# Kernel tuning notes

Hardware: AMD Instinct MI355X
Metric: run time of the kernel (lower is better)

The kernel has to match this reference:

```python
import jax, jax.numpy as jnp
import numpy as np

D_MODEL = 256
N_LAYER = 4
D_INNER = 512   # expand=2
D_STATE = 16
DT_RANK = 16    # ceil(d_model/16)
D_CONV = 4
VOCAB = 16
BATCH = 1
SEQLEN = 4096
EPS = 1e-5


def setup_inputs() -> dict:
    key = jax.random.key(0)
    ks = jax.random.split(key, 10)
    s = 0.02
    A_init = jnp.log(jnp.arange(1, D_STATE + 1, dtype=jnp.float32))  # S4D-real init
    return {
        "input_ids": jax.random.randint(ks[0], (BATCH, SEQLEN), 0, VOCAB, dtype=jnp.int32),
        "embed_w": jax.random.normal(ks[1], (VOCAB, D_MODEL), jnp.float32) * s,
        "norm_w": jnp.ones((N_LAYER, D_MODEL), jnp.float32),
        "in_proj_w": jax.random.normal(ks[2], (N_LAYER, 2 * D_INNER, D_MODEL), jnp.float32) * s,
        "out_proj_w": jax.random.normal(ks[3], (N_LAYER, D_MODEL, D_INNER), jnp.float32) * s,
        "conv_w": jax.random.normal(ks[4], (N_LAYER, 2, D_INNER, D_CONV), jnp.float32) * s,
        "conv_b": jnp.zeros((N_LAYER, 2, D_INNER), jnp.float32),
        "x_proj_w": jax.random.normal(ks[5], (N_LAYER, 2, DT_RANK + 2 * D_STATE, D_INNER), jnp.float32) * s,
        "dt_proj_w": jax.random.normal(ks[6], (N_LAYER, 2, D_INNER, DT_RANK), jnp.float32) * s,
        "dt_proj_b": jax.random.normal(ks[7], (N_LAYER, 2, D_INNER), jnp.float32) * 0.1,
        "A_log": jnp.broadcast_to(A_init, (N_LAYER, 2, D_INNER, D_STATE)) + 0.0,
        "Dp": jnp.ones((N_LAYER, 2, D_INNER), jnp.float32),
        "norm_f_w": jnp.ones((D_MODEL,), jnp.float32),
    }


def rmsnorm(x, w):
    return x * jax.lax.rsqrt(jnp.mean(x * x, axis=-1, keepdims=True) + EPS) * w


def selective_scan(u, dt, A, Bm, Cm, Dv):
    # u, dt: (B,L,Di); A: (Di,N); Bm, Cm: (B,L,N); Dv: (Di,)
    dA = jnp.exp(dt[..., None] * A)                         # (B,L,Di,N)
    dBu = dt[..., None] * Bm[:, :, None, :] * u[..., None]  # (B,L,Di,N)

    def step(h, xs):
        dA_t, dBu_t, C_t = xs
        h = dA_t * h + dBu_t                                # (B,Di,N)
        y = jnp.einsum('bdn,bn->bd', h, C_t)
        return h, y

    h0 = jnp.zeros((u.shape[0], D_INNER, D_STATE), u.dtype)
    xs = (jnp.moveaxis(dA, 1, 0), jnp.moveaxis(dBu, 1, 0), jnp.moveaxis(Cm, 1, 0))
    _, ys = jax.lax.scan(step, h0, xs)                      # (L,B,Di)
    return jnp.moveaxis(ys, 0, 1) + u * Dv


def mamba_dir(x, in_w, out_w, cw, cb, xpw, dtw, dtb, a_log, dv):
    # x: (B,L,D)
    xz = jnp.einsum('bld,ed->ble', x, in_w)                 # (B,L,2*Di)
    u, z = jnp.split(xz, 2, axis=-1)
    # causal depthwise conv1d
    uc = jnp.moveaxis(u, 1, 2)                              # (B,Di,L)
    uc = jax.lax.conv_general_dilated(
        uc, cw[:, None, :], (1,), [(D_CONV - 1, 0)],
        feature_group_count=D_INNER, dimension_numbers=('NCH', 'OIH', 'NCH'))
    u = jax.nn.silu(jnp.moveaxis(uc, 1, 2) + cb)            # (B,L,Di)
    xdb = jnp.einsum('bld,ed->ble', u, xpw)                 # (B,L,dt_rank+2N)
    dt_r, Bm, Cm = jnp.split(xdb, [DT_RANK, DT_RANK + D_STATE], axis=-1)
    dt = jax.nn.softplus(jnp.einsum('blr,dr->bld', dt_r, dtw) + dtb)
    A = -jnp.exp(a_log)                                     # (Di,N)
    y = selective_scan(u, dt, A, Bm, Cm, dv)
    y = y * jax.nn.silu(z)
    return jnp.einsum('bld,od->blo', y, out_w)


def reference(input_ids, embed_w, norm_w, in_proj_w, out_proj_w, conv_w, conv_b,
              x_proj_w, dt_proj_w, dt_proj_b, A_log, Dp, norm_f_w):
    h = embed_w[input_ids]                                  # (B,L,D)
    residual = None
    for i in range(N_LAYER):
        residual = h if residual is None else h + residual  # residual_in_fp32
        hn = rmsnorm(residual, norm_w[i])
        out_f = mamba_dir(hn, in_proj_w[i], out_proj_w[i], conv_w[i, 0], conv_b[i, 0],
                          x_proj_w[i, 0], dt_proj_w[i, 0], dt_proj_b[i, 0], A_log[i, 0], Dp[i, 0])
        out_r = mamba_dir(hn[:, ::-1], in_proj_w[i], out_proj_w[i], conv_w[i, 1], conv_b[i, 1],
                          x_proj_w[i, 1], dt_proj_w[i, 1], dt_proj_b[i, 1], A_log[i, 1], Dp[i, 1])[:, ::-1]
        h = out_f + out_r                                   # bidirectional 'add'
    residual = h + residual
    return rmsnorm(residual, norm_f_w)
```

## Files before the change

### kernel.cpp

```cpp
#include <hip/hip_runtime.h>
#include <hip/hip_bf16.h>
#include <math.h>

#define L_  4096
#define D_  256
#define DI_ 512
#define NS_ 16
#define NC_ 128
#define CH_ 32

typedef __attribute__((ext_vector_type(8))) short short8;
typedef __attribute__((ext_vector_type(4))) short short4v;
typedef __attribute__((ext_vector_type(4))) float f32x4;

__global__ __launch_bounds__(256) void prep_kernel(const int* __restrict__ ids,
    const float* __restrict__ ew, const float* __restrict__ inw,
    const float* __restrict__ outw, const float* __restrict__ xpw,
    float* __restrict__ res, __hip_bfloat16* __restrict__ inw_b,
    __hip_bfloat16* __restrict__ outw_b, __hip_bfloat16* __restrict__ xpw_b) {
  int idx = blockIdx.x * 256 + threadIdx.x;
  int l = idx >> 8, d = idx & 255;
  res[idx] = ew[ids[l] * D_ + d];
  inw_b[idx] = __float2bfloat16(inw[idx]);
  if (idx < 4 * 256 * 512)
    outw_b[idx] = __float2bfloat16(outw[idx]);
  if (idx < 4 * 2 * 64 * 512) {
    int layer = idx >> 16;
    int rem = idx & 65535;
    int dir = rem >> 15;
    int r = (rem >> 9) & 63, k = idx & 511;
    float v = (r < 48) ? xpw[(((size_t)layer * 2 + dir) * 48 + r) * 512 + k] : 0.f;
    xpw_b[idx] = __float2bfloat16(v);
  }
}

template<bool BF16OUT>
__global__ __launch_bounds__(256) void rmsnorm_kernel(float* __restrict__ residual,
    const float* __restrict__ h0, const float* __restrict__ h1,
    const float* __restrict__ w, void* __restrict__ out) {
  int row = blockIdx.x * 4 + (threadIdx.x >> 6);
  int lane = threadIdx.x & 63;
  size_t o = (size_t)row * D_ + lane * 4;
  float4 v = *(const float4*)(residual + o);
  if (h0) {
    float4 a = *(const float4*)(h0 + o);
    float4 b = *(const float4*)(h1 + o);
    v.x += a.x + b.x; v.y += a.y + b.y; v.z += a.z + b.z; v.w += a.w + b.w;
    *(float4*)(residual + o) = v;
  }
  float sq = fmaf(v.x, v.x, fmaf(v.y, v.y, fmaf(v.z, v.z, v.w * v.w)));
  #pragma unroll
  for (int s = 32; s > 0; s >>= 1) sq += __shfl_xor(sq, s, 64);
  float scale = rsqrtf(sq * (1.f / D_) + 1e-5f);
  float4 wv = *(const float4*)(w + lane * 4);
  float r0 = v.x * scale * wv.x, r1 = v.y * scale * wv.y;
  float r2 = v.z * scale * wv.z, r3 = v.w * scale * wv.w;
  if (BF16OUT) {
    __hip_bfloat16* ob = (__hip_bfloat16*)out + o;
    short4v s4;
    s4[0] = __bfloat16_as_short(__float2bfloat16(r0));
    s4[1] = __bfloat16_as_short(__float2bfloat16(r1));
    s4[2] = __bfloat16_as_short(__float2bfloat16(r2));
    s4[3] = __bfloat16_as_short(__float2bfloat16(r3));
    *reinterpret_cast<short4v*>(ob) = s4;
  } else {
    float4 r = {r0, r1, r2, r3};
    *((float4*)out + (o >> 2)) = r;
  }
}

__device__ __forceinline__ void gload_lds16(const void* g, void* l) {
  __builtin_amdgcn_global_load_lds((const __attribute__((address_space(1))) unsigned int*)g,
                                   (__attribute__((address_space(3))) unsigned int*)l,
                                   16, 0, 0);
}

template<int BM, int BN, bool BF16OUT>
__global__ __launch_bounds__(256) void gemm_bt_bf16(const __hip_bfloat16* __restrict__ A,
    const __hip_bfloat16* __restrict__ B, void* __restrict__ Cv, int M, int N, int K,
    size_t sA, size_t sB, size_t sC) {
  A += (size_t)blockIdx.z * sA; B += (size_t)blockIdx.z * sB;
  constexpr int FM = (BM / 2) / 16, FN = (BN / 2) / 16;
  constexpr int ABYTES = BM * 64, BBYTES = BN * 64;
  __shared__ __attribute__((aligned(16))) char As[ABYTES];
  __shared__ __attribute__((aligned(16))) char Bs[BBYTES];
  int tid = threadIdx.x, lane = tid & 63, w = tid >> 6;
  int bm = blockIdx.y * BM, bn = blockIdx.x * BN;
  int wr = (w >> 1) * (BM / 2), wc = (w & 1) * (BN / 2);
  f32x4 acc[FM][FN] = {};
  for (int k0 = 0; k0 < K; k0 += 32) {
    __syncthreads();
    #pragma unroll
    for (int i = 0; i < ABYTES / 4096; ++i) {
      int x = (i * 256 + tid) * 16;
      int xs = x ^ (((x >> 7) & 3) << 4);
      int row = xs >> 6, col = (xs & 63) >> 1;
      gload_lds16(A + (size_t)(bm + row) * K + k0 + col, As + i * 4096 + w * 1024);
    }
    if constexpr (ABYTES % 4096) {
      if (tid < (ABYTES % 4096) / 16) {
        int x = ((ABYTES / 4096) * 256 + tid) * 16;
        int xs = x ^ (((x >> 7) & 3) << 4);
        int row = xs >> 6, col = (xs & 63) >> 1;
        gload_lds16(A + (size_t)(bm + row) * K + k0 + col, As + (ABYTES / 4096) * 4096 + w * 1024);
      }
    }
    #pragma unroll
    for (int i = 0; i < BBYTES / 4096; ++i) {
      int x = (i * 256 + tid) * 16;
      int xs = x ^ (((x >> 7) & 3) << 4);
      int row = xs >> 6, col = (xs & 63) >> 1;
      gload_lds16(B + (size_t)(bn + row) * K + k0 + col, Bs + i * 4096 + w * 1024);
    }
    if constexpr (BBYTES % 4096) {
      if (tid < (BBYTES % 4096) / 16) {
        int x = ((BBYTES / 4096) * 256 + tid) * 16;
        int xs = x ^ (((x >> 7) & 3) << 4);
        int row = xs >> 6, col = (xs & 63) >> 1;
        gload_lds16(B + (size_t)(bn + row) * K + k0 + col, Bs + (BBYTES / 4096) * 4096 + w * 1024);
      }
    }
    __syncthreads();
    short8 af[FM], bf[FN];
    #pragma unroll
    for (int m = 0; m < FM; ++m) {
      int row = wr + m * 16 + (lane & 15);
      int x = row * 64 + ((lane >> 4) * 16);
      x ^= ((x >> 7) & 3) << 4;
      af[m] = *reinterpret_cast<const short8*>(As + x);
    }
    #pragma unroll
    for (int n = 0; n < FN; ++n) {
      int row = wc + n * 16 + (lane & 15);
      int x = row * 64 + ((lane >> 4) * 16);
      x ^= ((x >> 7) & 3) << 4;
      bf[n] = *reinterpret_cast<const short8*>(Bs + x);
    }
    #pragma unroll
    for (int m = 0; m < FM; ++m)
      #pragma unroll
      for (int n = 0; n < FN; ++n)
        acc[m][n] = __builtin_amdgcn_mfma_f32_16x16x32_bf16(af[m], bf[n], acc[m][n], 0, 0, 0);
  }
  #pragma unroll
  for (int m = 0; m < FM; ++m)
    #pragma unroll
    for (int n = 0; n < FN; ++n)
      #pragma unroll
      for (int j = 0; j < 4; ++j) {
        size_t off = (size_t)blockIdx.z * sC +
                     (size_t)(bm + wr + m * 16 + (lane >> 4) * 4 + j) * N + bn + wc + n * 16 + (lane & 15);
        if (BF16OUT) ((__hip_bfloat16*)Cv)[off] = __float2bfloat16(acc[m][n][j]);
        else         ((float*)Cv)[off] = acc[m][n][j];
      }
}

__global__ __launch_bounds__(256) void conv_silu_kernel(const __hip_bfloat16* __restrict__ xz,
    const float* __restrict__ cw, const float* __restrict__ cb,
    __hip_bfloat16* __restrict__ ucb) {
  int dir = blockIdx.y;
  int i8 = blockIdx.x * 256 + threadIdx.x;
  int l = i8 >> 6, d0 = (i8 & 63) * 8;
  const float* wp = cw + ((size_t)dir * DI_ + d0) * 4;
  float acc[8];
  #pragma unroll
  for (int j = 0; j < 8; ++j) acc[j] = cb[(size_t)dir * DI_ + d0 + j];
  #pragma unroll
  for (int k = 0; k < 4; ++k) {
    int lf = l - 3 + k;
    if (lf >= 0) {
      int pos = dir ? (L_ - 1 - lf) : lf;
      short8 xv = *reinterpret_cast<const short8*>(xz + (size_t)pos * 1024 + d0);
      #pragma unroll
      for (int j = 0; j < 8; ++j) {
        float xf = __uint_as_float((unsigned)(unsigned short)xv[j] << 16);
        acc[j] = fmaf(wp[j * 4 + k], xf, acc[j]);
      }
    }
  }
  short8 o8;
  #pragma unroll
  for (int j = 0; j < 8; ++j) {
    float s = acc[j] * __builtin_amdgcn_rcpf(1.f + __expf(-acc[j]));
    o8[j] = __bfloat16_as_short(__float2bfloat16(s));
  }
  *reinterpret_cast<short8*>(ucb + ((size_t)dir * L_ + l) * DI_ + d0) = o8;
}

__device__ __forceinline__ void scan_stage(int tid, int lane, int w, int q, int dir,
    const float* __restrict__ xdb, const __hip_bfloat16* __restrict__ uc,
    const float* __restrict__ dtw, const float* __restrict__ dtbp, int c,
    float (*sxdb)[64], unsigned short (*su)[128], float (*sdt)[128]) {
  const char* bg = (const char*)(xdb + ((size_t)dir * L_ + (size_t)c * CH_) * 64);
  const char* ug = (const char*)(uc + ((size_t)dir * L_ + (size_t)c * CH_) * DI_ + q * 128);
  #pragma unroll
  for (int i = 0; i < 2; ++i)
    gload_lds16(bg + w * 2048 + i * 1024 + lane * 16,
                (char*)sxdb + w * 2048 + i * 1024);
  #pragma unroll
  for (int i = 0; i < 2; ++i) {
    int unit = w * 128 + i * 64 + lane;
    int byte = unit * 16;
    gload_lds16(ug + (byte >> 8) * 1024 + (byte & 255),
                (char*)su + w * 2048 + i * 1024);
  }
  __syncthreads();
  int dlx = tid & 127, tst = tid >> 7;
  int dc = q * 128 + dlx;
  const float4* wr = (const float4*)(dtw + ((size_t)dir * DI_ + dc) * 16);
  float4 w0 = wr[0], w1 = wr[1], w2 = wr[2], w3 = wr[3];
  float bias = dtbp[(size_t)dir * DI_ + dc];
  #pragma unroll
  for (int i = 0; i < 16; ++i) {
    int t = tst + i * 2;
    const float4* xr = (const float4*)&sxdb[t][0];
    float4 x0 = xr[0], x1 = xr[1], x2 = xr[2], x3 = xr[3];
    float acc = bias;
    acc = fmaf(w0.x, x0.x, fmaf(w0.y, x0.y, fmaf(w0.z, x0.z, fmaf(w0.w, x0.w, acc))));
    acc = fmaf(w1.x, x1.x, fmaf(w1.y, x1.y, fmaf(w1.z, x1.z, fmaf(w1.w, x1.w, acc))));
    acc = fmaf(w2.x, x2.x, fmaf(w2.y, x2.y, fmaf(w2.z, x2.z, fmaf(w2.w, x2.w, acc))));
    acc = fmaf(w3.x, x3.x, fmaf(w3.y, x3.y, fmaf(w3.z, x3.z, fmaf(w3.w, x3.w, acc))));
    float e = __expf(fminf(acc, 20.f));
    sdt[t][dlx] = acc > 20.f ? acc : __logf(1.f + e);
  }
  __syncthreads();
}

__global__ __launch_bounds__(256) void scan_pass1(const __hip_bfloat16* __restrict__ uc,
    const float* __restrict__ xdb, const float* __restrict__ dtw,
    const float* __restrict__ dtbp, const float* __restrict__ A_log,
    float* __restrict__ Pb, float* __restrict__ Qb) {
  int dir = blockIdx.y;
  int c = blockIdx.x >> 2, q = blockIdx.x & 3;
  int tid = threadIdx.x, lane = tid & 63, w = tid >> 6;
  int dl = tid >> 1, nh = tid & 1;
  int d = q * 128 + dl;
  __shared__ __attribute__((aligned(16))) float sxdb[CH_][64];
  __shared__ __attribute__((aligned(16))) unsigned short su[CH_][128];
  __shared__ __attribute__((aligned(16))) float sdt[CH_][128];
  float Av[8], P[8], Q[8];
  const float4* Ab4 = (const float4*)(A_log + ((size_t)dir * DI_ + d) * 16 + nh * 8);
  float4 a0 = Ab4[0], a1 = Ab4[1];
  float al[8] = {a0.x, a0.y, a0.z, a0.w, a1.x, a1.y, a1.z, a1.w};
  #pragma unroll
  for (int j = 0; j < 8; ++j) { Av[j] = -__expf(al[j]); P[j] = 1.f; Q[j] = 0.f; }
  scan_stage(tid, lane, w, q, dir, xdb, uc, dtw, dtbp, c, sxdb, su, sdt);
  #pragma unroll 2
  for (int t = 0; t < CH_; ++t) {
    float dtv = sdt[t][dl];
    float uv  = __uint_as_float((unsigned)su[t][dl] << 16);
    float du = dtv * uv;
    const float4* Br = (const float4*)&sxdb[t][16 + nh * 8];
    float4 b0 = Br[0], b1 = Br[1];
    float bb[8] = {b0.x, b0.y, b0.z, b0.w, b1.x, b1.y, b1.z, b1.w};
    #pragma unroll
    for (int j = 0; j < 8; ++j) {
      float dA = __expf(dtv * Av[j]);
      P[j] *= dA;
      Q[j] = fmaf(dA, Q[j], bb[j] * du);
    }
  }
  size_t ob = ((size_t)dir * NC_ + c) * 8192 + (size_t)(nh * 8) * 512 + d;
  #pragma unroll
  for (int j = 0; j < 8; ++j) { Pb[ob + j * 512] = P[j]; Qb[ob + j * 512] = Q[j]; }
}

__global__ __launch_bounds__(64) void scan_combine(const float* __restrict__ Pb,
    const float* __restrict__ Qb, float* __restrict__ H0) {
  int idx = blockIdx.x * 64 + threadIdx.x;
  int dir = idx >> 13; int s = idx & 8191;
  size_t base = (size_t)dir * NC_ * 8192 + s;
  float h = 0.f;
  #pragma unroll 8
  for (int c = 0; c < NC_; ++c) {
    size_t o = base + (size_t)c * 8192;
    H0[o] = h;
    h = fmaf(Pb[o], h, Qb[o]);
  }
}

__global__ __launch_bounds__(256) void scan_pass2(const __hip_bfloat16* __restrict__ uc,
    const float* __restrict__ xdb, const float* __restrict__ dtw,
    const float* __restrict__ dtbp, const float* __restrict__ A_log,
    const float* __restrict__ Dp, const __hip_bfloat16* __restrict__ xz,
    const float* __restrict__ H0, __hip_bfloat16* __restrict__ yg) {
  int dir = blockIdx.y;
  int c = blockIdx.x >> 2, q = blockIdx.x & 3;
  int tid = threadIdx.x, lane = tid & 63, w = tid >> 6;
  int dl = tid >> 1, nh = tid & 1;
  int d = q * 128 + dl;
  __shared__ __attribute__((aligned(16))) float sxdb[CH_][64];
  __shared__ __attribute__((aligned(16))) unsigned short su[CH_][128];
  __shared__ __attribute__((aligned(16))) float sdt[CH_][128];
  float Av[8], h[8];
  const float4* Ab4 = (const float4*)(A_log + ((size_t)dir * DI_ + d) * 16 + nh * 8);
  float4 a0 = Ab4[0], a1 = Ab4[1];
  float al[8] = {a0.x, a0.y, a0.z, a0.w, a1.x, a1.y, a1.z, a1.w};
  size_t ob = ((size_t)dir * NC_ + c) * 8192 + (size_t)(nh * 8) * 512 + d;
  #pragma unroll
  for (int j = 0; j < 8; ++j) { Av[j] = -__expf(al[j]); h[j] = H0[ob + j * 512]; }
  float Dv = Dp[(size_t)dir * DI_ + d];
  scan_stage(tid, lane, w, q, dir, xdb, uc, dtw, dtbp, c, sxdb, su, sdt);
  #pragma unroll 2
  for (int t = 0; t < CH_; ++t) {
    float dtv = sdt[t][dl];
    float uv  = __uint_as_float((unsigned)su[t][dl] << 16);
    float du = dtv * uv;
    const float4* Br = (const float4*)&sxdb[t][16 + nh * 8];
    const float4* Cr = (const float4*)&sxdb[t][32 + nh * 8];
    float4 b0 = Br[0], b1 = Br[1], c0 = Cr[0], c1 = Cr[1];
    float bb[8] = {b0.x, b0.y, b0.z, b0.w, b1.x, b1.y, b1.z, b1.w};
    float cc[8] = {c0.x, c0.y, c0.z, c0.w, c1.x, c1.y, c1.z, c1.w};
    float y = 0.f;
    #pragma unroll
    for (int j = 0; j < 8; ++j) {
      float dA = __expf(dtv * Av[j]);
      h[j] = fmaf(dA, h[j], bb[j] * du);
      y = fmaf(h[j], cc[j], y);
    }
    y += __shfl_xor(y, 1, 64);
    if (nh == 0) {
      int l = c * CH_ + t;
      int pos = dir ? (L_ - 1 - l) : l;
      float zv = __bfloat162float(xz[(size_t)pos * 1024 + DI_ + d]);
      float g = zv * __builtin_amdgcn_rcpf(1.f + __expf(-zv));
      yg[((size_t)dir * L_ + pos) * DI_ + d] = __float2bfloat16((y + uv * Dv) * g);
    }
  }
}

extern "C" void kernel_launch(void* const* d_in, const int* in_sizes, int n_in,
                              void* d_out, int out_size, void* d_ws, size_t ws_size,
                              hipStream_t stream) {
  const int*   ids       = (const int*)  d_in[0];
  const float* embed_w   = (const float*)d_in[1];
  const float* norm_w    = (const float*)d_in[2];
  const float* in_proj_w = (const float*)d_in[3];
  const float* out_proj_w= (const float*)d_in[4];
  const float* conv_w    = (const float*)d_in[5];
  const float* conv_b    = (const float*)d_in[6];
  const float* x_proj_w  = (const float*)d_in[7];
  const float* dt_proj_w = (const float*)d_in[8];
  const float* dt_proj_b = (const float*)d_in[9];
  const float* A_log     = (const float*)d_in[10];
  const float* Dp        = (const float*)d_in[11];
  const float* norm_f_w  = (const float*)d_in[12];

  float* ws = (float*)d_ws;
  float* residual = ws; ws += (size_t)L_ * D_;
  float* xdb      = ws; ws += (size_t)2 * L_ * 64;
  float* hbuf2    = ws; ws += (size_t)2 * L_ * D_;
  float* Pb       = ws; ws += (size_t)2 * NC_ * 8192;
  float* Qb       = ws; ws += (size_t)2 * NC_ * 8192;
  float* H0       = ws; ws += (size_t)2 * NC_ * 8192;
  __hip_bfloat16* hn_b   = (__hip_bfloat16*)ws;
  __hip_bfloat16* xz_b   = hn_b + (size_t)L_ * D_;
  __hip_bfloat16* yg_b   = xz_b + (size_t)L_ * 1024;
  __hip_bfloat16* uc_b   = yg_b + (size_t)2 * L_ * DI_;
  __hip_bfloat16* inw_b  = uc_b + (size_t)2 * L_ * DI_;
  __hip_bfloat16* outw_b = inw_b + (size_t)4 * 1024 * D_;
  __hip_bfloat16* xpw_b  = outw_b + (size_t)4 * D_ * DI_;

  prep_kernel<<<L_ * D_ / 256, 256, 0, stream>>>(ids, embed_w, in_proj_w, out_proj_w,
                                                 x_proj_w, residual, inw_b, outw_b, xpw_b);

  for (int i = 0; i < 4; ++i) {
    rmsnorm_kernel<true><<<L_ / 4, 256, 0, stream>>>(
        residual, i ? hbuf2 : nullptr, i ? hbuf2 + (size_t)L_ * D_ : nullptr,
        norm_w + (size_t)i * D_, hn_b);
    gemm_bt_bf16<64, 64, true><<<dim3(1024 / 64, L_ / 64, 1), 256, 0, stream>>>(
        hn_b, inw_b + (size_t)i * 1024 * D_, xz_b, L_, 1024, D_, 0, 0, 0);
    conv_silu_kernel<<<dim3(L_ * DI_ / 8 / 256, 2), 256, 0, stream>>>(
        xz_b, conv_w + (size_t)i * 2 * DI_ * 4, conv_b + (size_t)i * 2 * DI_, uc_b);
    gemm_bt_bf16<32, 64, false><<<dim3(1, L_ / 32, 2), 256, 0, stream>>>(
        uc_b, xpw_b + (size_t)i * 2 * 64 * DI_, xdb, L_, 64, DI_,
        (size_t)L_ * DI_, (size_t)64 * DI_, (size_t)L_ * 64);
    dim3 gsc(NC_ * 4, 2);
    scan_pass1<<<gsc, 256, 0, stream>>>(
        uc_b, xdb, dt_proj_w + (size_t)i * 2 * DI_ * 16, dt_proj_b + (size_t)i * 2 * DI_,
        A_log + (size_t)i * 2 * DI_ * NS_, Pb, Qb);
    scan_combine<<<256, 64, 0, stream>>>(Pb, Qb, H0);
    scan_pass2<<<gsc, 256, 0, stream>>>(
        uc_b, xdb, dt_proj_w + (size_t)i * 2 * DI_ * 16, dt_proj_b + (size_t)i * 2 * DI_,
        A_log + (size_t)i * 2 * DI_ * NS_, Dp + (size_t)i * 2 * DI_,
        xz_b, H0, yg_b);
    gemm_bt_bf16<64, 64, false><<<dim3(D_ / 64, L_ / 64, 2), 256, 0, stream>>>(
        yg_b, outw_b + (size_t)i * D_ * DI_, hbuf2, L_, D_, DI_,
        (size_t)L_ * DI_, 0, (size_t)L_ * D_);
  }

  rmsnorm_kernel<false><<<L_ / 4, 256, 0, stream>>>(
      residual, hbuf2, hbuf2 + (size_t)L_ * D_, norm_f_w, d_out);
}
```

Before: 509.2 us.

## Fuse bidirectional out_proj into single K=1024 GEMM and enlarge in_proj tile

The forward and reverse scan outputs are now interleaved per position into a single L x 1024 buffer. The out_proj weight is duplicated along K, so one GEMM with K=1024 produces the summed bidirectional output directly. This removes the second fp32 output buffer and the extra add in rmsnorm, cutting memory traffic and one batch of GEMM launches. The in_proj GEMM tile also grows to 128 rows, which reduces the grid size and increases reuse at the cost of fewer blocks.

```diff
diff --git a/kernel.cpp b/kernel.cpp
--- a/kernel.cpp
+++ b/kernel.cpp
@@ -22,8 +22,12 @@
   int l = idx >> 8, d = idx & 255;
   res[idx] = ew[ids[l] * D_ + d];
   inw_b[idx] = __float2bfloat16(inw[idx]);
-  if (idx < 4 * 256 * 512)
-    outw_b[idx] = __float2bfloat16(outw[idx]);
+  {
+    int layer = idx >> 18;
+    int rem = idx & 262143;
+    int o = rem >> 10, k = rem & 1023;
+    outw_b[idx] = __float2bfloat16(outw[((size_t)layer * 256 + o) * 512 + (k & 511)]);
+  }
   if (idx < 4 * 2 * 64 * 512) {
     int layer = idx >> 16;
     int rem = idx & 65535;
@@ -36,16 +40,14 @@
 
 template<bool BF16OUT>
 __global__ __launch_bounds__(256) void rmsnorm_kernel(float* __restrict__ residual,
-    const float* __restrict__ h0, const float* __restrict__ h1,
-    const float* __restrict__ w, void* __restrict__ out) {
+    const float* __restrict__ hadd, const float* __restrict__ w, void* __restrict__ out) {
   int row = blockIdx.x * 4 + (threadIdx.x >> 6);
   int lane = threadIdx.x & 63;
   size_t o = (size_t)row * D_ + lane * 4;
   float4 v = *(const float4*)(residual + o);
-  if (h0) {
-    float4 a = *(const float4*)(h0 + o);
-    float4 b = *(const float4*)(h1 + o);
-    v.x += a.x + b.x; v.y += a.y + b.y; v.z += a.z + b.z; v.w += a.w + b.w;
+  if (hadd) {
+    float4 a = *(const float4*)(hadd + o);
+    v.x += a.x; v.y += a.y; v.z += a.z; v.w += a.w;
     *(float4*)(residual + o) = v;
   }
   float sq = fmaf(v.x, v.x, fmaf(v.y, v.y, fmaf(v.z, v.z, v.w * v.w)));
@@ -324,7 +326,7 @@
       int pos = dir ? (L_ - 1 - l) : l;
       float zv = __bfloat162float(xz[(size_t)pos * 1024 + DI_ + d]);
       float g = zv * __builtin_amdgcn_rcpf(1.f + __expf(-zv));
-      yg[((size_t)dir * L_ + pos) * DI_ + d] = __float2bfloat16((y + uv * Dv) * g);
+      yg[(size_t)pos * 1024 + (size_t)dir * DI_ + d] = __float2bfloat16((y + uv * Dv) * g);
     }
   }
 }
@@ -349,26 +351,25 @@
   float* ws = (float*)d_ws;
   float* residual = ws; ws += (size_t)L_ * D_;
   float* xdb      = ws; ws += (size_t)2 * L_ * 64;
-  float* hbuf2    = ws; ws += (size_t)2 * L_ * D_;
+  float* hbuf     = ws; ws += (size_t)L_ * D_;
   float* Pb       = ws; ws += (size_t)2 * NC_ * 8192;
   float* Qb       = ws; ws += (size_t)2 * NC_ * 8192;
   float* H0       = ws; ws += (size_t)2 * NC_ * 8192;
   __hip_bfloat16* hn_b   = (__hip_bfloat16*)ws;
   __hip_bfloat16* xz_b   = hn_b + (size_t)L_ * D_;
   __hip_bfloat16* yg_b   = xz_b + (size_t)L_ * 1024;
-  __hip_bfloat16* uc_b   = yg_b + (size_t)2 * L_ * DI_;
+  __hip_bfloat16* uc_b   = yg_b + (size_t)L_ * 1024;
   __hip_bfloat16* inw_b  = uc_b + (size_t)2 * L_ * DI_;
   __hip_bfloat16* outw_b = inw_b + (size_t)4 * 1024 * D_;
-  __hip_bfloat16* xpw_b  = outw_b + (size_t)4 * D_ * DI_;
+  __hip_bfloat16* xpw_b  = outw_b + (size_t)4 * D_ * 1024;
 
   prep_kernel<<<L_ * D_ / 256, 256, 0, stream>>>(ids, embed_w, in_proj_w, out_proj_w,
                                                  x_proj_w, residual, inw_b, outw_b, xpw_b);
 
   for (int i = 0; i < 4; ++i) {
-    rmsnorm_kernel<true><<<L_ / 4, 256, 0, stream>>>(
-        residual, i ? hbuf2 : nullptr, i ? hbuf2 + (size_t)L_ * D_ : nullptr,
-        norm_w + (size_t)i * D_, hn_b);
-    gemm_bt_bf16<64, 64, true><<<dim3(1024 / 64, L_ / 64, 1), 256, 0, stream>>>(
+    rmsnorm_kernel<true><<<L_ / 4, 256, 0, stream>>>(residual, i ? hbuf : nullptr,
+                                                     norm_w + (size_t)i * D_, hn_b);
+    gemm_bt_bf16<128, 64, true><<<dim3(1024 / 64, L_ / 128, 1), 256, 0, stream>>>(
         hn_b, inw_b + (size_t)i * 1024 * D_, xz_b, L_, 1024, D_, 0, 0, 0);
     conv_silu_kernel<<<dim3(L_ * DI_ / 8 / 256, 2), 256, 0, stream>>>(
         xz_b, conv_w + (size_t)i * 2 * DI_ * 4, conv_b + (size_t)i * 2 * DI_, uc_b);
@@ -384,11 +385,9 @@
         uc_b, xdb, dt_proj_w + (size_t)i * 2 * DI_ * 16, dt_proj_b + (size_t)i * 2 * DI_,
         A_log + (size_t)i * 2 * DI_ * NS_, Dp + (size_t)i * 2 * DI_,
         xz_b, H0, yg_b);
-    gemm_bt_bf16<64, 64, false><<<dim3(D_ / 64, L_ / 64, 2), 256, 0, stream>>>(
-        yg_b, outw_b + (size_t)i * D_ * DI_, hbuf2, L_, D_, DI_,
-        (size_t)L_ * DI_, 0, (size_t)L_ * D_);
-  }
-
-  rmsnorm_kernel<false><<<L_ / 4, 256, 0, stream>>>(
-      residual, hbuf2, hbuf2 + (size_t)L_ * D_, norm_f_w, d_out);
-}
+    gemm_bt_bf16<64, 64, false><<<dim3(D_ / 64, L_ / 64, 1), 256, 0, stream>>>(
+        yg_b, outw_b + (size_t)i * D_ * 1024, hbuf, L_, D_, 1024, 0, 0, 0);
+  }
+
+  rmsnorm_kernel<false><<<L_ / 4, 256, 0, stream>>>(residual, hbuf, norm_f_w, d_out);
+}
```

New measurement: 537.0 us. +5.5%, slower.
